# Performance work log

Measured on AMD Instinct MI355X. Metric: run time of the kernel, lower is better.

Reference implementation:

```python
import jax, jax.numpy as jnp
import numpy as np

N, K, D = 8192, 512, 4096

def setup_inputs() -> dict:
    key = jax.random.key(0)
    k1, k2, k3 = jax.random.split(key, 3)
    features = jax.random.normal(k1, (N, K), dtype=jnp.float32)
    w = jax.random.normal(k2, (D, N), dtype=jnp.float32)
    E = jax.random.normal(k3, (K, D), dtype=jnp.float32) / np.sqrt(K)  # embed_matrix (k x d)
    b = jnp.zeros((D,), dtype=jnp.float32)  # bias initialized to zeros in the module
    return {"features": features, "w": w, "E": E, "b": b}

def reference(features, w, E, b):
    # Linear: y = features @ E + b  -> (N, D)   (torch weight is E.mT, so x @ W.T == x @ E)
    y = features @ E + b
    # diag(y @ w): equivalent to row-wise dot products, same math without the NxN matmul
    return jnp.einsum("nd,dn->n", y, w)
```

## Files before the change

kernel.cpp:

```cpp
#include <hip/hip_runtime.h>

#define N_DIM 8192
#define K_DIM 512
#define D_DIM 4096

typedef __bf16 bf16x8 __attribute__((ext_vector_type(8)));
typedef float  f32x16 __attribute__((ext_vector_type(16)));
typedef unsigned short u16x8 __attribute__((ext_vector_type(8)));

__device__ __forceinline__ unsigned short f2bf(float f) {
    union { float f; unsigned int u; } v; v.f = f;
    unsigned int r = v.u + 0x7FFF + ((v.u >> 16) & 1);
    return (unsigned short)(r >> 16);
}

__global__ __launch_bounds__(256) void transpose_E(const float* __restrict__ E,
                                                   unsigned short* __restrict__ ET) {
    __shared__ float tile[64][65];
    const int d0 = blockIdx.x * 64;
    const int k0 = blockIdx.y * 64;
    const int tid = threadIdx.x;
    const int r  = tid / 16;
    const int c4 = (tid % 16) * 4;
#pragma unroll
    for (int p = 0; p < 4; ++p) {
        int k = p * 16 + r;
        float4 v = *reinterpret_cast<const float4*>(E + (size_t)(k0 + k) * D_DIM + d0 + c4);
        tile[k][c4 + 0] = v.x; tile[k][c4 + 1] = v.y;
        tile[k][c4 + 2] = v.z; tile[k][c4 + 3] = v.w;
    }
    __syncthreads();
#pragma unroll
    for (int p = 0; p < 4; ++p) {
        int d = p * 16 + r;
        ushort4 o;
        o.x = f2bf(tile[c4 + 0][d]);
        o.y = f2bf(tile[c4 + 1][d]);
        o.z = f2bf(tile[c4 + 2][d]);
        o.w = f2bf(tile[c4 + 3][d]);
        *reinterpret_cast<ushort4*>(ET + (size_t)(d0 + d) * K_DIM + k0 + c4) = o;
    }
}

__global__ __launch_bounds__(256) void convert_F(const float* __restrict__ F,
                                                 unsigned short* __restrict__ FB) {
    const int idx8 = (blockIdx.x * 256 + threadIdx.x) * 8;
    float4 a = *reinterpret_cast<const float4*>(F + idx8);
    float4 b = *reinterpret_cast<const float4*>(F + idx8 + 4);
    u16x8 o;
    o[0] = f2bf(a.x); o[1] = f2bf(a.y); o[2] = f2bf(a.z); o[3] = f2bf(a.w);
    o[4] = f2bf(b.x); o[5] = f2bf(b.y); o[6] = f2bf(b.z); o[7] = f2bf(b.w);
    *reinterpret_cast<u16x8*>(FB + idx8) = o;
}

__global__ __launch_bounds__(256) void gemm_fused(const unsigned short* __restrict__ FB,
                                                  const float* __restrict__ W,
                                                  const unsigned short* __restrict__ ET,
                                                  const float* __restrict__ B,
                                                  float* __restrict__ out) {
    __shared__ unsigned short Ash[2 * 128 * 32];
    __shared__ unsigned short Bsh[2 * 128 * 32];

    const int tid  = threadIdx.x;
    const int wave = tid >> 6;
    const int lane = tid & 63;
    const int wy   = wave >> 1;
    const int wx   = wave & 1;
    const int l31  = lane & 31;
    const int half = lane >> 5;

    const int f   = blockIdx.x + ((int)gridDim.x) * blockIdx.y;
    const int xcd = f & 7;
    const int s   = f >> 3;
    const int ntile = (xcd & 3) * 16 + (s & 15);
    const int dtile = (xcd >> 2) * 16 + (s >> 4);
    const int n0 = ntile * 128;
    const int d0 = dtile * 128;

    f32x16 acc[2][2] = {};

    const int srow   = lane >> 2;
    const int schunk = (((lane & 3) ^ ((srow >> 1) & 3)) * 8);

    for (int kt = 0; kt < K_DIM / 64; ++kt) {
        const int kb = kt * 64;
#pragma unroll
        for (int p = 0; p < 2; ++p) {
#pragma unroll
            for (int jj = 0; jj < 2; ++jj) {
                const int j = wave * 2 + jj;
                const unsigned short* ga =
                    ET + (size_t)(d0 + j * 16 + srow) * K_DIM + kb + p * 32 + schunk;
                __builtin_amdgcn_global_load_lds(
                    (const __attribute__((address_space(1))) void*)ga,
                    (__attribute__((address_space(3))) void*)(Ash + p * 4096 + j * 512),
                    16, 0, 0);
                const unsigned short* gb =
                    FB + (size_t)(n0 + j * 16 + srow) * K_DIM + kb + p * 32 + schunk;
                __builtin_amdgcn_global_load_lds(
                    (const __attribute__((address_space(1))) void*)gb,
                    (__attribute__((address_space(3))) void*)(Bsh + p * 4096 + j * 512),
                    16, 0, 0);
            }
        }
        __syncthreads();

#pragma unroll
        for (int ks = 0; ks < 4; ++ks) {
            const int p = ks >> 1;
            const int c = (ks & 1) * 2 + half;
            bf16x8 af[2], bf[2];
#pragma unroll
            for (int mi = 0; mi < 2; ++mi) {
                const int R = wy * 64 + mi * 32 + l31;
                const int slot = c ^ ((R >> 1) & 3);
                af[mi] = *reinterpret_cast<const bf16x8*>(
                    Ash + p * 4096 + R * 32 + slot * 8);
            }
#pragma unroll
            for (int ni = 0; ni < 2; ++ni) {
                const int R = wx * 64 + ni * 32 + l31;
                const int slot = c ^ ((R >> 1) & 3);
                bf[ni] = *reinterpret_cast<const bf16x8*>(
                    Bsh + p * 4096 + R * 32 + slot * 8);
            }
#pragma unroll
            for (int mi = 0; mi < 2; ++mi)
#pragma unroll
                for (int ni = 0; ni < 2; ++ni)
                    acc[mi][ni] = __builtin_amdgcn_mfma_f32_32x32x16_bf16(
                        af[mi], bf[ni], acc[mi][ni], 0, 0, 0);
        }
        __syncthreads();
    }

    const int nb = n0 + wx * 64;
    float part0 = 0.f, part1 = 0.f;
#pragma unroll
    for (int mi = 0; mi < 2; ++mi) {
        const int dbase = d0 + wy * 64 + mi * 32 + 4 * half;
#pragma unroll
        for (int reg = 0; reg < 16; ++reg) {
            const int dd = dbase + (reg & 3) + 8 * (reg >> 2);
            const float bd = B[dd];
            const float* wr = W + (size_t)dd * N_DIM + nb;
            part0 += (acc[mi][0][reg] + bd) * __builtin_nontemporal_load(wr + l31);
            part1 += (acc[mi][1][reg] + bd) * __builtin_nontemporal_load(wr + 32 + l31);
        }
    }
    part0 += __shfl_xor(part0, 32);
    part1 += __shfl_xor(part1, 32);
    if (lane < 32) {
        atomicAdd(out + nb + l31, part0);
        atomicAdd(out + nb + 32 + l31, part1);
    }
}

extern "C" void kernel_launch(void* const* d_in, const int* in_sizes, int n_in,
                              void* d_out, int out_size, void* d_ws, size_t ws_size,
                              hipStream_t stream) {
    const float* F = (const float*)d_in[0];
    const float* W = (const float*)d_in[1];
    const float* E = (const float*)d_in[2];
    const float* B = (const float*)d_in[3];
    float* out = (float*)d_out;

    unsigned short* ET = (unsigned short*)d_ws;
    unsigned short* FB = (unsigned short*)((char*)d_ws + (size_t)D_DIM * K_DIM * 2);

    hipMemsetAsync(d_out, 0, (size_t)out_size * sizeof(float), stream);
    transpose_E<<<dim3(D_DIM / 64, K_DIM / 64), 256, 0, stream>>>(E, ET);
    convert_F<<<dim3(N_DIM * K_DIM / (256 * 8)), 256, 0, stream>>>(F, FB);
    gemm_fused<<<dim3(N_DIM / 128, D_DIM / 128), 256, 0, stream>>>(FB, W, ET, B, out);
}
```

Baseline: 236.3 us.

## Prefetch W tile into LDS at kernel start to overlap with GEMM mainloop

The 128x128 fp32 tile of W is now loaded asynchronously into LDS with global-to-LDS loads issued before the K loop, so its fetch overlaps the MFMA main loop instead of being read directly from global memory in the epilogue. To fit LDS (64KB for W), the A/B staging is cut from a K-step of 64 to 32, doubling the number of loop iterations and barriers, and launch bounds request two blocks per CU. There is no explicit wait on the W loads before the epilogue; it relies on the in-loop barriers and waitcnt draining them. Halving the K-step adds synchronization overhead per unit of work.

```diff
diff --git a/kernel.cpp b/kernel.cpp
--- a/kernel.cpp
+++ b/kernel.cpp
@@ -53,13 +53,14 @@
     *reinterpret_cast<u16x8*>(FB + idx8) = o;
 }
 
-__global__ __launch_bounds__(256) void gemm_fused(const unsigned short* __restrict__ FB,
-                                                  const float* __restrict__ W,
-                                                  const unsigned short* __restrict__ ET,
-                                                  const float* __restrict__ B,
-                                                  float* __restrict__ out) {
-    __shared__ unsigned short Ash[2 * 128 * 32];
-    __shared__ unsigned short Bsh[2 * 128 * 32];
+__global__ __launch_bounds__(256, 2) void gemm_fused(const unsigned short* __restrict__ FB,
+                                                     const float* __restrict__ W,
+                                                     const unsigned short* __restrict__ ET,
+                                                     const float* __restrict__ B,
+                                                     float* __restrict__ out) {
+    __shared__ unsigned short Ash[128 * 32];
+    __shared__ unsigned short Bsh[128 * 32];
+    __shared__ float          Wsh[128 * 128];
 
     const int tid  = threadIdx.x;
     const int wave = tid >> 6;
@@ -77,75 +78,84 @@
     const int n0 = ntile * 128;
     const int d0 = dtile * 128;
 
+    {
+        const int drow2 = lane >> 5;
+        const int nc    = (lane & 31) * 4;
+#pragma unroll
+        for (int i = 0; i < 16; ++i) {
+            const int dr = wave * 32 + i * 2;
+            const float* gw = W + (size_t)(d0 + dr + drow2) * N_DIM + n0 + nc;
+            __builtin_amdgcn_global_load_lds(
+                (const __attribute__((address_space(1))) void*)gw,
+                (__attribute__((address_space(3))) void*)(Wsh + dr * 128),
+                16, 0, 2 );
+        }
+    }
+
     f32x16 acc[2][2] = {};
 
     const int srow   = lane >> 2;
     const int schunk = (((lane & 3) ^ ((srow >> 1) & 3)) * 8);
 
-    for (int kt = 0; kt < K_DIM / 64; ++kt) {
-        const int kb = kt * 64;
+    for (int kt = 0; kt < K_DIM / 32; ++kt) {
+        const int kb = kt * 32;
 #pragma unroll
-        for (int p = 0; p < 2; ++p) {
-#pragma unroll
-            for (int jj = 0; jj < 2; ++jj) {
-                const int j = wave * 2 + jj;
-                const unsigned short* ga =
-                    ET + (size_t)(d0 + j * 16 + srow) * K_DIM + kb + p * 32 + schunk;
-                __builtin_amdgcn_global_load_lds(
-                    (const __attribute__((address_space(1))) void*)ga,
-                    (__attribute__((address_space(3))) void*)(Ash + p * 4096 + j * 512),
-                    16, 0, 0);
-                const unsigned short* gb =
-                    FB + (size_t)(n0 + j * 16 + srow) * K_DIM + kb + p * 32 + schunk;
-                __builtin_amdgcn_global_load_lds(
-                    (const __attribute__((address_space(1))) void*)gb,
-                    (__attribute__((address_space(3))) void*)(Bsh + p * 4096 + j * 512),
-                    16, 0, 0);
-            }
+        for (int jj = 0; jj < 2; ++jj) {
+            const int j = wave * 2 + jj;
+            const unsigned short* ga =
+                ET + (size_t)(d0 + j * 16 + srow) * K_DIM + kb + schunk;
+            __builtin_amdgcn_global_load_lds(
+                (const __attribute__((address_space(1))) void*)ga,
+                (__attribute__((address_space(3))) void*)(Ash + j * 512),
+                16, 0, 0);
+            const unsigned short* gb =
+                FB + (size_t)(n0 + j * 16 + srow) * K_DIM + kb + schunk;
+            __builtin_amdgcn_global_load_lds(
+                (const __attribute__((address_space(1))) void*)gb,
+                (__attribute__((address_space(3))) void*)(Bsh + j * 512),
+                16, 0, 0);
         }
         __syncthreads();
 
 #pragma unroll
-        for (int ks = 0; ks < 4; ++ks) {
-            const int p = ks >> 1;
-            const int c = (ks & 1) * 2 + half;
-            bf16x8 af[2], bf[2];
+        for (int ks = 0; ks < 2; ++ks) {
+            const int c = ks * 2 + half;
+            bf16x8 af[2], bfr[2];
 #pragma unroll
             for (int mi = 0; mi < 2; ++mi) {
                 const int R = wy * 64 + mi * 32 + l31;
                 const int slot = c ^ ((R >> 1) & 3);
-                af[mi] = *reinterpret_cast<const bf16x8*>(
-                    Ash + p * 4096 + R * 32 + slot * 8);
+                af[mi] = *reinterpret_cast<const bf16x8*>(Ash + R * 32 + slot * 8);
             }
 #pragma unroll
             for (int ni = 0; ni < 2; ++ni) {
                 const int R = wx * 64 + ni * 32 + l31;
                 const int slot = c ^ ((R >> 1) & 3);
-                bf[ni] = *reinterpret_cast<const bf16x8*>(
-                    Bsh + p * 4096 + R * 32 + slot * 8);
+                bfr[ni] = *reinterpret_cast<const bf16x8*>(Bsh + R * 32 + slot * 8);
             }
 #pragma unroll
             for (int mi = 0; mi < 2; ++mi)
 #pragma unroll
                 for (int ni = 0; ni < 2; ++ni)
                     acc[mi][ni] = __builtin_amdgcn_mfma_f32_32x32x16_bf16(
-                        af[mi], bf[ni], acc[mi][ni], 0, 0, 0);
+                        af[mi], bfr[ni], acc[mi][ni], 0, 0, 0);
         }
         __syncthreads();
     }
 
-    const int nb = n0 + wx * 64;
+    const int nbl = wx * 64;
+    const int nb  = n0 + nbl;
     float part0 = 0.f, part1 = 0.f;
 #pragma unroll
     for (int mi = 0; mi < 2; ++mi) {
-        const int dbase = d0 + wy * 64 + mi * 32 + 4 * half;
+        const int dlb = wy * 64 + mi * 32 + 4 * half;
 #pragma unroll
         for (int reg = 0; reg < 16; ++reg) {
-            const int dd = dbase + (reg & 3) + 8 * (reg >> 2);
-            const float bd = B[dd];
-            const float* wr = W + (size_t)dd * N_DIM + nb;
-            part0 += (acc[mi][0][reg] + bd) * __builtin_nontemporal_load(wr + l31);
-            part1 += (acc[mi][1][reg] + bd) * __builtin_nontemporal_load(wr + 32 + l31);
+            const int dl = dlb + (reg & 3) + 8 * (reg >> 2);
+            const float bd = B[d0 + dl];
+            const float* wr = Wsh + dl * 128 + nbl;
+            part0 += (acc[mi][0][reg] + bd) * wr[l31];
+            part1 += (acc[mi][1][reg] + bd) * wr[32 + l31];
         }
     }
     part0 += __shfl_xor(part0, 32);
```

After: 243.5 us. 3.0% more time.
